# Performance work log

Hardware: AMD Instinct MI355X
Metric: run time of the kernel (lower is better)

The kernel has to match this reference:

```python
import jax, jax.numpy as jnp
import numpy as np

N_NODES = 100000
N_EDGES = 3200000
IN_CH = 768
OUT_CH = 64
NEG_SLOPE = 0.2  # GATv2 default leaky_relu negative_slope


def setup_inputs() -> dict:
    key = jax.random.key(0)
    ks = jax.random.split(key, 9)
    node = jax.random.normal(ks[0], (N_NODES, IN_CH), dtype=jnp.float32)
    edge_index = jax.random.randint(ks[1], (2, N_EDGES), 0, N_NODES, dtype=jnp.int64)
    s = 0.02
    return {
        "node": node,
        "edge_index": edge_index,
        # GATv2Conv params (heads=1, share_weights=False)
        "W_l": jax.random.normal(ks[2], (IN_CH, OUT_CH), dtype=jnp.float32) * s,
        "b_l": jnp.zeros((OUT_CH,), dtype=jnp.float32),
        "W_r": jax.random.normal(ks[3], (IN_CH, OUT_CH), dtype=jnp.float32) * s,
        "b_r": jnp.zeros((OUT_CH,), dtype=jnp.float32),
        "att": jax.random.normal(ks[4], (OUT_CH,), dtype=jnp.float32) * s,
        "gnn_bias": jnp.zeros((OUT_CH,), dtype=jnp.float32),
        # parallel Linear branch
        "W_lin": jax.random.normal(ks[5], (IN_CH, OUT_CH), dtype=jnp.float32) * s,
        "b_lin": jnp.zeros((OUT_CH,), dtype=jnp.float32),
    }


def reference(node, edge_index, W_l, b_l, W_r, b_r, att, gnn_bias, W_lin, b_lin):
    N = node.shape[0]
    # add self loops
    loops = jnp.arange(N, dtype=edge_index.dtype)
    src = jnp.concatenate([edge_index[0], loops])  # message source j
    dst = jnp.concatenate([edge_index[1], loops])  # aggregation target i

    x_l = node @ W_l + b_l  # [N, C] source transform
    x_r = node @ W_r + b_r  # [N, C] target transform

    # GATv2 edge scores: a^T LeakyReLU(x_l[j] + x_r[i])
    e = jax.nn.leaky_relu(x_l[src] + x_r[dst], NEG_SLOPE) @ att  # [E]

    # segment softmax over edges grouped by destination
    m = jax.ops.segment_max(e, dst, num_segments=N)  # self loops -> no empty segments
    p = jnp.exp(e - m[dst])
    denom = jax.ops.segment_sum(p, dst, num_segments=N)
    alpha = p / denom[dst]  # [E]

    # weighted scatter-add aggregation of source messages
    out = jax.ops.segment_sum(alpha[:, None] * x_l[src], dst, num_segments=N)
    out = out + gnn_bias

    # parallel linear branch + ReLU (dropout = identity in eval mode)
    out = out + node @ W_lin + b_lin
    return jax.nn.relu(out)
```

## Files before the change

kernel.cpp:

```cpp
#include <hip/hip_runtime.h>
#include <hip/hip_bf16.h>

#define NN 100000
#define NE 3200000
#define KD 768

#define BW 128
#define NBUK 782
#define CAPB 4608
#define CHUNK 8192

typedef __bf16 bf16;
typedef __bf16 bf16x8 __attribute__((ext_vector_type(8)));
typedef float f32x4 __attribute__((ext_vector_type(4)));

__global__ void k_detect(const int* __restrict__ ei, int* __restrict__ meta) {
    if (blockIdx.x == 0 && threadIdx.x == 0) {
        int odd_or = 0;
        for (int t = 0; t < 16; ++t) odd_or |= ei[2 * t + 1];
        meta[0] = (odd_or == 0) ? 2 : 1;
    }
}

__global__ void k_trans(const float* __restrict__ Wl, const float* __restrict__ Wr,
                        const float* __restrict__ Wlin, bf16* __restrict__ BT) {
    int t = blockIdx.x * 256 + threadIdx.x;
    if (t >= 192 * KD) return;
    int n = t / KD, k = t % KD;
    const float* W = (n < 64) ? Wl : (n < 128) ? Wr : Wlin;
    BT[t] = (bf16)W[k * 64 + (n & 63)];
}

__global__ __launch_bounds__(256) void k_gemm(
    const float* __restrict__ node, const bf16* __restrict__ BT,
    const float* __restrict__ bl, const float* __restrict__ br,
    const float* __restrict__ blin, const float* __restrict__ gbias,
    bf16* __restrict__ xl, bf16* __restrict__ xr, float* __restrict__ base) {
    int wave = threadIdx.x >> 6, lane = threadIdx.x & 63;
    int quad = lane >> 4, l16 = lane & 15;
    int r0 = blockIdx.x * 128 + wave * 32;

    f32x4 acc[2][12] = {};
    long a0 = (long)((r0 + l16 < NN) ? r0 + l16 : NN - 1) * KD;
    long a1 = (long)((r0 + 16 + l16 < NN) ? r0 + 16 + l16 : NN - 1) * KD;

    for (int kt = 0; kt < KD; kt += 32) {
        int kk = kt + quad * 8;
        float4 p00 = *(const float4*)(node + a0 + kk);
        float4 p01 = *(const float4*)(node + a0 + kk + 4);
        float4 p10 = *(const float4*)(node + a1 + kk);
        float4 p11 = *(const float4*)(node + a1 + kk + 4);
        bf16x8 af0, af1;
        af0[0]=(bf16)p00.x; af0[1]=(bf16)p00.y; af0[2]=(bf16)p00.z; af0[3]=(bf16)p00.w;
        af0[4]=(bf16)p01.x; af0[5]=(bf16)p01.y; af0[6]=(bf16)p01.z; af0[7]=(bf16)p01.w;
        af1[0]=(bf16)p10.x; af1[1]=(bf16)p10.y; af1[2]=(bf16)p10.z; af1[3]=(bf16)p10.w;
        af1[4]=(bf16)p11.x; af1[5]=(bf16)p11.y; af1[6]=(bf16)p11.z; af1[7]=(bf16)p11.w;
#pragma unroll
        for (int nf = 0; nf < 12; ++nf) {
            bf16x8 bfr = *(const bf16x8*)(BT + (nf * 16 + l16) * KD + kk);
            acc[0][nf] = __builtin_amdgcn_mfma_f32_16x16x32_bf16(af0, bfr, acc[0][nf], 0, 0, 0);
            acc[1][nf] = __builtin_amdgcn_mfma_f32_16x16x32_bf16(af1, bfr, acc[1][nf], 0, 0, 0);
        }
    }
#pragma unroll
    for (int rf = 0; rf < 2; ++rf)
#pragma unroll
        for (int nf = 0; nf < 12; ++nf)
#pragma unroll
            for (int i = 0; i < 4; ++i) {
                int row = r0 + rf * 16 + quad * 4 + i;
                int gcol = nf * 16 + l16;
                if (row >= NN) continue;
                float v = acc[rf][nf][i];
                if (gcol < 64) {
                    xl[row * 64 + gcol] = (bf16)(v + bl[gcol]);
                } else if (gcol < 128) {
                    int c = gcol - 64;
                    xr[row * 64 + c] = (bf16)(v + br[c]);
                } else {
                    int c = gcol - 128;
                    base[row * 64 + c] = v + blin[c] + gbias[c];
                }
            }
}

__global__ __launch_bounds__(1024) void k_bucket(
    const int* __restrict__ ei, const int* __restrict__ meta,
    int* __restrict__ gcnt, int* __restrict__ gstore) {
    __shared__ int hist[NBUK], excl[NBUK], lcur[NBUK], gbase[NBUK];
    __shared__ int sorted[CHUNK];
    __shared__ int wsum[16], wexcl[17];
    int tid = threadIdx.x, wv = tid >> 6, ln = tid & 63;
    long e0 = (long)blockIdx.x * CHUNK;
    int nedge = (int)(((long)NE - e0) < CHUNK ? ((long)NE - e0) : CHUNK);
    int st = meta[0];

    for (int k = tid; k < NBUK; k += 1024) hist[k] = 0;
    __syncthreads();
    for (int k = tid; k < nedge; k += 1024) {
        int d = ei[(size_t)NE * st + (size_t)(e0 + k) * st];
        atomicAdd(&hist[d >> 7], 1);
    }
    __syncthreads();
    {
        int v = (tid < NBUK) ? hist[tid] : 0;
        int s = v;
#pragma unroll
        for (int off = 1; off < 64; off <<= 1) {
            int t = __shfl_up(s, off, 64);
            if (ln >= off) s += t;
        }
        if (ln == 63) wsum[wv] = s;
        __syncthreads();
        if (wv == 0 && ln < 16) {
            int ws = wsum[ln];
#pragma unroll
            for (int off = 1; off < 16; off <<= 1) {
                int t = __shfl_up(ws, off, 64);
                if (ln >= off) ws += t;
            }
            wexcl[ln + 1] = ws;
            if (ln == 0) wexcl[0] = 0;
        }
        __syncthreads();
        if (tid < NBUK) {
            int ex = wexcl[wv] + s - v;
            excl[tid] = ex;
            lcur[tid] = ex;
        }
    }
    for (int k = tid; k < NBUK; k += 1024) {
        int c = hist[k];
        gbase[k] = c ? atomicAdd(&gcnt[k], c) : 0;
    }
    __syncthreads();
    for (int k = tid; k < nedge; k += 1024) {
        int s = ei[(size_t)(e0 + k) * st];
        int d = ei[(size_t)NE * st + (size_t)(e0 + k) * st];
        int pos = atomicAdd(&lcur[d >> 7], 1);
        sorted[pos] = (s << 7) | (d & 127);
    }
    __syncthreads();
    for (int b = wv; b < NBUK; b += 16) {
        int cnt = hist[b], lo = excl[b], gb = gbase[b];
        for (int k = ln; k < cnt; k += 64) {
            int gp = gb + k;
            if (gp < CAPB) gstore[(size_t)b * CAPB + gp] = sorted[lo + k];
        }
    }
}

__global__ __launch_bounds__(1024) void k_agg2(
    const bf16* __restrict__ xl, const bf16* __restrict__ xr,
    const float* __restrict__ att, const int* __restrict__ gcnt,
    const int* __restrict__ gstore, float* __restrict__ out) {
    __shared__ int raw[CAPB], srt[CAPB];
    __shared__ int rp[BW + 1], cur[BW], h[BW];
    int b = blockIdx.x, tid = threadIdx.x;
    int len = gcnt[b]; if (len > CAPB) len = CAPB;

    if (tid < BW) h[tid] = 0;
    __syncthreads();
    for (int k = tid; k < len; k += 1024) {
        int p = gstore[(size_t)b * CAPB + k];
        raw[k] = p;
        atomicAdd(&h[p & 127], 1);
    }
    __syncthreads();
    if (tid < 64) {
        int a0 = h[tid], a1 = h[64 + tid];
        int s0 = a0, s1 = a1;
#pragma unroll
        for (int off = 1; off < 64; off <<= 1) {
            int t0 = __shfl_up(s0, off, 64);
            int t1 = __shfl_up(s1, off, 64);
            if (tid >= off) { s0 += t0; s1 += t1; }
        }
        int tot0 = __shfl(s0, 63, 64);
        rp[tid + 1] = s0;
        rp[65 + tid] = s1 + tot0;
        if (tid == 0) rp[0] = 0;
    }
    __syncthreads();
    if (tid < BW) cur[tid] = rp[tid];
    __syncthreads();
    for (int k = tid; k < len; k += 1024) {
        int p = raw[k];
        int pos = atomicAdd(&cur[p & 127], 1);
        srt[pos] = p >> 7;
    }
    __syncthreads();

    int wv = tid >> 6, lane = tid & 63;
    int quad = lane >> 4, l16 = lane & 15;
    float att_c = att[lane];
    bf16x8 b_lo, b_hi;
#pragma unroll
    for (int j = 0; j < 8; ++j) {
        b_lo[j] = (bf16)att[quad * 8 + j];
        b_hi[j] = (bf16)att[32 + quad * 8 + j];
    }
    for (int dl = wv; dl < BW; dl += 16) {
        int i = b * BW + dl;
        if (i >= NN) break;
        float xr_c = (float)xr[(size_t)i * 64 + lane];
        float xl_c = (float)xl[(size_t)i * 64 + lane];
        bf16x8 xr_lo = *(const bf16x8*)(xr + (size_t)i * 64 + quad * 8);
        bf16x8 xr_hi = *(const bf16x8*)(xr + (size_t)i * 64 + 32 + quad * 8);

        float s = xl_c + xr_c;
        float v = att_c * (s > 0.f ? s : 0.2f * s);
#pragma unroll
        for (int m = 32; m; m >>= 1) v += __shfl_xor(v, m, 64);
        float p0 = __expf(v);
        float denom = p0;
        float accv = p0 * xl_c;

        int beg = rp[dl], end = rp[dl + 1];
        for (int eb = beg; eb < end; eb += 16) {
            int idx = eb + l16;
            int jc = srt[(idx < end) ? idx : beg];
            bf16x8 a_lo = *(const bf16x8*)(xl + (size_t)jc * 64 + quad * 8);
            bf16x8 a_hi = *(const bf16x8*)(xl + (size_t)jc * 64 + 32 + quad * 8);
            bf16x8 f_lo, f_hi;
#pragma unroll
            for (int j = 0; j < 8; ++j) {
                float a = (float)a_lo[j] + (float)xr_lo[j];
                f_lo[j] = (bf16)(a > 0.f ? a : 0.2f * a);
                float b2 = (float)a_hi[j] + (float)xr_hi[j];
                f_hi[j] = (bf16)(b2 > 0.f ? b2 : 0.2f * b2);
            }
            f32x4 sc = {0.f, 0.f, 0.f, 0.f};
            sc = __builtin_amdgcn_mfma_f32_16x16x32_bf16(f_lo, b_lo, sc, 0, 0, 0);
            sc = __builtin_amdgcn_mfma_f32_16x16x32_bf16(f_hi, b_hi, sc, 0, 0, 0);
            float p[4];
#pragma unroll
            for (int r = 0; r < 4; ++r) {
                float pe = __expf(sc[r]);
                p[r] = (eb + quad * 4 + r < end) ? pe : 0.f;
            }
#pragma unroll
            for (int t = 0; t < 16; ++t) {
                float pt = __shfl(p[t & 3], (t >> 2) * 16, 64);
                int jj = __shfl(jc, t, 64);
                float xlv = (float)xl[(size_t)jj * 64 + lane];
                denom += pt;
                accv += pt * xlv;
            }
        }
        float o = accv / denom + out[(size_t)i * 64 + lane];
        out[(size_t)i * 64 + lane] = (o > 0.f ? o : 0.f);
    }
}

extern "C" void kernel_launch(void* const* d_in, const int* in_sizes, int n_in,
                              void* d_out, int out_size, void* d_ws, size_t ws_size,
                              hipStream_t stream) {
    const float* node = (const float*)d_in[0];
    const int* ei     = (const int*)d_in[1];
    const float* Wl   = (const float*)d_in[2];
    const float* bl   = (const float*)d_in[3];
    const float* Wr   = (const float*)d_in[4];
    const float* br   = (const float*)d_in[5];
    const float* attv = (const float*)d_in[6];
    const float* gb   = (const float*)d_in[7];
    const float* Wlin = (const float*)d_in[8];
    const float* blin = (const float*)d_in[9];
    float* out = (float*)d_out;

    char* w = (char*)d_ws;
    bf16* xl    = (bf16*)w;   w += (size_t)NN * 64 * 2;
    bf16* xr    = (bf16*)w;   w += (size_t)NN * 64 * 2;
    bf16* BT    = (bf16*)w;   w += (size_t)192 * KD * 2;
    int* meta   = (int*)w;    w += 64;
    int* gcnt   = (int*)w;    w += (size_t)NBUK * 4 + 64;
    int* gstore = (int*)w;    w += (size_t)NBUK * CAPB * 4;

    hipMemsetAsync(gcnt, 0, (size_t)NBUK * 4, stream);
    k_detect<<<1, 64, 0, stream>>>(ei, meta);
    k_trans<<<(192 * KD + 255) / 256, 256, 0, stream>>>(Wl, Wr, Wlin, BT);
    k_gemm<<<(NN + 127) / 128, 256, 0, stream>>>(node, BT, bl, br, blin, gb, xl, xr, out);
    k_bucket<<<(NE + CHUNK - 1) / CHUNK, 1024, 0, stream>>>(ei, meta, gcnt, gstore);
    k_agg2<<<NBUK, 1024, 0, stream>>>(xl, xr, attv, gcnt, gstore, out);
}
```

Baseline: 803.3 us.

## Split GEMM columns across waves, prefetch next A tile, raise occupancy

The node-projection GEMM now gives each block 64 rows, with waves split 2x2 over rows and over the 192 output columns, so each wave holds 2x6 accumulators instead of 2x12. It also register-prefetches the next k-step of node fp32 data before the MFMAs, and adds a launch-bounds occupancy hint of 4. The aim is to cut register pressure so more waves fit per CU, and to hide global load latency on the memory-bound read of the 300MB node matrix. In exchange, each node row is now loaded by two waves instead of one, which doubles A-side requests, though L2 may absorb the repeat.

```diff
diff --git a/kernel.cpp b/kernel.cpp
--- a/kernel.cpp
+++ b/kernel.cpp
@@ -31,45 +31,60 @@
     BT[t] = (bf16)W[k * 64 + (n & 63)];
 }
 
-__global__ __launch_bounds__(256) void k_gemm(
+__device__ __forceinline__ bf16x8 cvt8(float4 a, float4 b) {
+    bf16x8 r;
+    r[0] = (bf16)a.x; r[1] = (bf16)a.y; r[2] = (bf16)a.z; r[3] = (bf16)a.w;
+    r[4] = (bf16)b.x; r[5] = (bf16)b.y; r[6] = (bf16)b.z; r[7] = (bf16)b.w;
+    return r;
+}
+
+__global__ __launch_bounds__(256, 4) void k_gemm(
     const float* __restrict__ node, const bf16* __restrict__ BT,
     const float* __restrict__ bl, const float* __restrict__ br,
     const float* __restrict__ blin, const float* __restrict__ gbias,
     bf16* __restrict__ xl, bf16* __restrict__ xr, float* __restrict__ base) {
     int wave = threadIdx.x >> 6, lane = threadIdx.x & 63;
     int quad = lane >> 4, l16 = lane & 15;
-    int r0 = blockIdx.x * 128 + wave * 32;
-
-    f32x4 acc[2][12] = {};
+    int r0 = blockIdx.x * 64 + (wave & 1) * 32;
+    int c0 = (wave >> 1) * 96;
+
+    f32x4 acc[2][6] = {};
     long a0 = (long)((r0 + l16 < NN) ? r0 + l16 : NN - 1) * KD;
     long a1 = (long)((r0 + 16 + l16 < NN) ? r0 + 16 + l16 : NN - 1) * KD;
+    int kq = quad * 8;
+
+    float4 c00 = *(const float4*)(node + a0 + kq);
+    float4 c01 = *(const float4*)(node + a0 + kq + 4);
+    float4 c10 = *(const float4*)(node + a1 + kq);
+    float4 c11 = *(const float4*)(node + a1 + kq + 4);
 
     for (int kt = 0; kt < KD; kt += 32) {
-        int kk = kt + quad * 8;
-        float4 p00 = *(const float4*)(node + a0 + kk);
-        float4 p01 = *(const float4*)(node + a0 + kk + 4);
-        float4 p10 = *(const float4*)(node + a1 + kk);
-        float4 p11 = *(const float4*)(node + a1 + kk + 4);
-        bf16x8 af0, af1;
-        af0[0]=(bf16)p00.x; af0[1]=(bf16)p00.y; af0[2]=(bf16)p00.z; af0[3]=(bf16)p00.w;
-        af0[4]=(bf16)p01.x; af0[5]=(bf16)p01.y; af0[6]=(bf16)p01.z; af0[7]=(bf16)p01.w;
-        af1[0]=(bf16)p10.x; af1[1]=(bf16)p10.y; af1[2]=(bf16)p10.z; af1[3]=(bf16)p10.w;
-        af1[4]=(bf16)p11.x; af1[5]=(bf16)p11.y; af1[6]=(bf16)p11.z; af1[7]=(bf16)p11.w;
-#pragma unroll
-        for (int nf = 0; nf < 12; ++nf) {
-            bf16x8 bfr = *(const bf16x8*)(BT + (nf * 16 + l16) * KD + kk);
+        int kkn = ((kt + 32 < KD) ? kt + 32 : 0) + kq;
+        float4 n00 = *(const float4*)(node + a0 + kkn);
+        float4 n01 = *(const float4*)(node + a0 + kkn + 4);
+        float4 n10 = *(const float4*)(node + a1 + kkn);
+        float4 n11 = *(const float4*)(node + a1 + kkn + 4);
+
+        bf16x8 af0 = cvt8(c00, c01);
+        bf16x8 af1 = cvt8(c10, c11);
+        int kk = kt + kq;
+        const bf16* bp = BT + (size_t)(c0 + l16) * KD + kk;
+#pragma unroll
+        for (int nf = 0; nf < 6; ++nf) {
+            bf16x8 bfr = *(const bf16x8*)(bp + (size_t)nf * 16 * KD);
             acc[0][nf] = __builtin_amdgcn_mfma_f32_16x16x32_bf16(af0, bfr, acc[0][nf], 0, 0, 0);
             acc[1][nf] = __builtin_amdgcn_mfma_f32_16x16x32_bf16(af1, bfr, acc[1][nf], 0, 0, 0);
         }
+        c00 = n00; c01 = n01; c10 = n10; c11 = n11;
     }
 #pragma unroll
     for (int rf = 0; rf < 2; ++rf)
 #pragma unroll
-        for (int nf = 0; nf < 12; ++nf)
+        for (int nf = 0; nf < 6; ++nf)
 #pragma unroll
             for (int i = 0; i < 4; ++i) {
                 int row = r0 + rf * 16 + quad * 4 + i;
-                int gcol = nf * 16 + l16;
+                int gcol = c0 + nf * 16 + l16;
                 if (row >= NN) continue;
                 float v = acc[rf][nf][i];
                 if (gcol < 64) {
@@ -279,7 +294,7 @@
     hipMemsetAsync(gcnt, 0, (size_t)NBUK * 4, stream);
     k_detect<<<1, 64, 0, stream>>>(ei, meta);
     k_trans<<<(192 * KD + 255) / 256, 256, 0, stream>>>(Wl, Wr, Wlin, BT);
-    k_gemm<<<(NN + 127) / 128, 256, 0, stream>>>(node, BT, bl, br, blin, gb, xl, xr, out);
+    k_gemm<<<(NN + 63) / 64, 256, 0, stream>>>(node, BT, bl, br, blin, gb, xl, xr, out);
     k_bucket<<<(NE + CHUNK - 1) / CHUNK, 1024, 0, stream>>>(ei, meta, gcnt, gstore);
     k_agg2<<<NBUK, 1024, 0, stream>>>(xl, xr, attv, gcnt, gstore, out);
 }
```

Result: no change. 810.6 us (+0.9%).
